# Optimization experiments

Hardware: AMD Instinct MI355X
Metric: run time of the kernel (lower is better)

The kernel has to match this reference:

```python
import jax, jax.numpy as jnp
import numpy as np

B, N, M, D, H, DFF = 1, 2048, 2048, 1024, 16, 4096
MASK_VAL = -50000.0
EPS = 1e-5


def _xavier(k, shape):
    lim = np.sqrt(6.0 / (shape[0] + shape[1])).astype(np.float32)
    return jax.random.uniform(k, shape, jnp.float32, -lim, lim)


def setup_inputs() -> dict:
    key = jax.random.key(0)
    ks = jax.random.split(key, 8)
    return {
        "x": jax.random.normal(ks[0], (B, N, D), jnp.float32),
        "context": jax.random.normal(ks[1], (B, M, D), jnp.float32),
        "Wq": _xavier(ks[2], (D, D)), "bq": jnp.zeros((D,), jnp.float32),
        "Wkv": _xavier(ks[3], (D, 2 * D)), "bkv": jnp.zeros((2 * D,), jnp.float32),
        "Wo": _xavier(ks[4], (D, D)), "bo": jnp.zeros((D,), jnp.float32),
        "ln1_g": jnp.ones((D,), jnp.float32), "ln1_b": jnp.zeros((D,), jnp.float32),
        "W1": _xavier(ks[5], (D, DFF)), "bf1": jnp.zeros((DFF,), jnp.float32),
        "W2": _xavier(ks[6], (DFF, D)), "bf2": jnp.zeros((D,), jnp.float32),
        "ln2_g": jnp.ones((D,), jnp.float32), "ln2_b": jnp.zeros((D,), jnp.float32),
    }


def _layernorm(x, g, b):
    mu = x.mean(-1, keepdims=True)
    var = ((x - mu) ** 2).mean(-1, keepdims=True)
    return (x - mu) * jax.lax.rsqrt(var + EPS) * g + b


def reference(x, context, Wq, bq, Wkv, bkv, Wo, bo, ln1_g, ln1_b, W1, bf1, W2, bf2, ln2_g, ln2_b):
    b, n, d = x.shape
    m = context.shape[1]
    h = H
    dh = d // h
    scale = dh ** -0.5
    # q from x only; k,v from [x; context]
    q = (x @ Wq + bq).reshape(b, n, h, dh).transpose(0, 2, 1, 3)          # b h n dh
    kv_in = jnp.concatenate([x, context], axis=1)                          # b (n+m) d
    k, v = jnp.split(kv_in @ Wkv + bkv, 2, axis=-1)
    k = k.reshape(b, n + m, h, dh).transpose(0, 2, 1, 3)                   # b h (n+m) dh
    v = v.reshape(b, n + m, h, dh).transpose(0, 2, 1, 3)
    dots = jnp.einsum('bhid,bhjd->bhij', q * scale, k)                     # b h n (n+m)
    # causal mask applies only to the self-attention (first n) key columns
    rows = jnp.arange(n)[:, None]
    cols = jnp.arange(n + m)[None, :]
    causal = (cols < n) & (cols > rows)
    dots = jnp.where(causal, MASK_VAL, dots)
    attn = jax.nn.softmax(dots, axis=-1)                                   # dropout = identity (eval)
    out = jnp.einsum('bhij,bhjd->bhid', attn, v)
    out = out.transpose(0, 2, 1, 3).reshape(b, n, d) @ Wo + bo
    # PostNorm(Residual(attn))
    x1 = _layernorm(x + out, ln1_g, ln1_b)
    # PostNorm(Residual(FFN)) with exact-erf GELU
    ff = jax.nn.gelu(x1 @ W1 + bf1, approximate=False) @ W2 + bf2
    return _layernorm(x1 + ff, ln2_g, ln2_b)
```

## Files before the change

kernel.cpp:

```cpp
#include <hip/hip_runtime.h>


using bf16x8 = __attribute__((ext_vector_type(8))) short;
using f32x4  = __attribute__((ext_vector_type(4))) float;

__device__ __forceinline__ ushort f2bf(float f) {
    unsigned u = __float_as_uint(f);
    unsigned r = (u + 0x7fffu + ((u >> 16) & 1u)) >> 16;
    return (ushort)r;
}

__device__ __forceinline__ void gload16(const void* g, void* l) {
    __builtin_amdgcn_global_load_lds(
        (const __attribute__((address_space(1))) void*)g,
        (__attribute__((address_space(3))) void*)l, 16, 0, 0);
}

__device__ __forceinline__ float gelu_erf(float v) {
    return 0.5f * v * (1.0f + erff(v * 0.70710678118654752f));
}

__global__ __launch_bounds__(256) void cvt4(const float* __restrict__ in,
                                            ushort* __restrict__ out, int n) {
    int i = (blockIdx.x * 256 + threadIdx.x) * 4;
    if (i + 3 < n) {
        float4 v = *(const float4*)(in + i);
        ushort4 o;
        o.x = f2bf(v.x); o.y = f2bf(v.y); o.z = f2bf(v.z); o.w = f2bf(v.w);
        *(ushort4*)(out + i) = o;
    }
}

__global__ __launch_bounds__(256) void tcvt(const float* __restrict__ in,
                                            ushort* __restrict__ out, int R, int C) {
    __shared__ float tile[32][33];
    const int tx = threadIdx.x, ty = threadIdx.y;
    const int c0 = blockIdx.x * 32, r0 = blockIdx.y * 32;
#pragma unroll
    for (int i = 0; i < 4; ++i)
        tile[ty + 8 * i][tx] = in[(size_t)(r0 + ty + 8 * i) * C + c0 + tx];
    __syncthreads();
#pragma unroll
    for (int i = 0; i < 4; ++i)
        out[(size_t)(c0 + ty + 8 * i) * R + r0 + tx] = f2bf(tile[tx][ty + 8 * i]);
}

__global__ __launch_bounds__(256) void vtrans(const ushort* __restrict__ KV,
                                              ushort* __restrict__ Vt) {
    __shared__ ushort tile[32][34];
    const int tx = threadIdx.x, ty = threadIdx.y;
    const int j0 = blockIdx.x * 32, d0 = blockIdx.y * 32;
#pragma unroll
    for (int i = 0; i < 4; ++i)
        tile[ty + 8 * i][tx] = KV[(size_t)(j0 + ty + 8 * i) * 2048 + 1024 + d0 + tx];
    __syncthreads();
#pragma unroll
    for (int i = 0; i < 4; ++i)
        Vt[(size_t)(d0 + ty + 8 * i) * 4096 + j0 + tx] = tile[tx][ty + 8 * i];
}

template <int BM, int BN, int ACT, int OUTF32, int RES, int SCALED, int SPLITK>
__global__ __launch_bounds__(256) void gemm_bt(
    const ushort* __restrict__ A, int lda, const ushort* __restrict__ Bt, int ldb,
    const float* __restrict__ bias, const float* __restrict__ resid,
    void* __restrict__ Cout, int M, int N, int K, float scale) {
    constexpr int MR = BM / 32, NR = BN / 32;
    __shared__ __align__(16) ushort Asm[BM * 64];
    __shared__ __align__(16) ushort Bsm[BN * 64];
    const int tid = threadIdx.x;
    const int w = tid >> 6, lane = tid & 63, g = lane >> 4, i15 = lane & 15;
    const int wm = w >> 1, wn = w & 1;
    const int m0 = blockIdx.y * BM, n0 = blockIdx.x * BN;
    if (SPLITK) {
        A += (size_t)blockIdx.z * K;
        Bt += (size_t)blockIdx.z * K;
    }

    f32x4 acc[MR][NR] = {};

    for (int kt = 0; kt < K; kt += 64) {
#pragma unroll
        for (int q = 0; q < BM / 32; ++q) {
            int off = (w * (BM / 32) + q) * 1024 + lane * 16;
            int r = off >> 7, cb = off & 127;
            int scb = cb ^ ((r & 7) << 4);
            const void* src = (const char*)A + ((size_t)(m0 + r) * lda + kt) * 2 + scb;
            gload16(src, (char*)Asm + (w * (BM / 32) + q) * 1024);
        }
#pragma unroll
        for (int q = 0; q < BN / 32; ++q) {
            int off = (w * (BN / 32) + q) * 1024 + lane * 16;
            int r = off >> 7, cb = off & 127;
            int scb = cb ^ ((r & 7) << 4);
            const void* src = (const char*)Bt + ((size_t)(n0 + r) * ldb + kt) * 2 + scb;
            gload16(src, (char*)Bsm + (w * (BN / 32) + q) * 1024);
        }
        __syncthreads();

#pragma unroll
        for (int kc = 0; kc < 2; ++kc) {
            bf16x8 af[MR], bfr[NR];
#pragma unroll
            for (int mi = 0; mi < MR; ++mi) {
                int r = wm * (BM / 2) + mi * 16 + i15;
                af[mi] = *(const bf16x8*)((const char*)Asm + r * 128 +
                                          ((kc * 64 + g * 16) ^ ((r & 7) << 4)));
            }
#pragma unroll
            for (int ni = 0; ni < NR; ++ni) {
                int r = wn * (BN / 2) + ni * 16 + i15;
                bfr[ni] = *(const bf16x8*)((const char*)Bsm + r * 128 +
                                           ((kc * 64 + g * 16) ^ ((r & 7) << 4)));
            }
#pragma unroll
            for (int mi = 0; mi < MR; ++mi)
#pragma unroll
                for (int ni = 0; ni < NR; ++ni)
                    acc[mi][ni] = __builtin_amdgcn_mfma_f32_16x16x32_bf16(
                        af[mi], bfr[ni], acc[mi][ni], 0, 0, 0);
        }
        __syncthreads();
    }

    float* Cf = (float*)Cout;
    if (SPLITK) Cf += (size_t)blockIdx.z * M * N;

#pragma unroll
    for (int ni = 0; ni < NR; ++ni) {
        int col = n0 + wn * (BN / 2) + ni * 16 + i15;
        float bb = bias ? bias[col] : 0.f;
#pragma unroll
        for (int mi = 0; mi < MR; ++mi) {
#pragma unroll
            for (int r2 = 0; r2 < 4; ++r2) {
                int row = m0 + wm * (BM / 2) + mi * 16 + 4 * g + r2;
                float v = acc[mi][ni][r2] + bb;
                if (ACT) v = gelu_erf(v);
                if (SCALED) v *= scale;
                size_t off = (size_t)row * N + col;
                if (OUTF32) {
                    float rv = RES ? resid[off] : 0.f;
                    Cf[off] = v + rv;
                } else {
                    ((ushort*)Cout)[off] = f2bf(v);
                }
            }
        }
    }
}

template <int SPLIT>
__global__ __launch_bounds__(256) void flash_attn(
    const ushort* __restrict__ Q,
    const ushort* __restrict__ KVb,
    const ushort* __restrict__ Vt,
    ushort* __restrict__ O,
    float* __restrict__ Opart,
    float* __restrict__ Ml) {
    constexpr int D = 1024;
    __shared__ __align__(16) ushort Ksm[2][64 * 64];
    __shared__ __align__(16) ushort Vsm[2][64 * 64];
    __shared__ __align__(16) ushort Psm[4][16 * 64];

    const int tid = threadIdx.x;
    const int w = tid >> 6, lane = tid & 63, g = lane >> 4, i15 = lane & 15;
    const int bid = blockIdx.x;
    const int h = bid & 15;
    int qi, s;
    if (SPLIT) { qi = 31 - ((bid >> 4) >> 1); s = (bid >> 4) & 1; }
    else       { qi = 31 - (bid >> 4); s = 0; }
    const int qb = qi * 64;
    const int qrow = qb + w * 16 + i15;

    bf16x8 qf[2];
    qf[0] = *(const bf16x8*)(Q + (size_t)qrow * D + h * 64 + g * 8);
    qf[1] = *(const bf16x8*)(Q + (size_t)qrow * D + h * 64 + 32 + g * 8);

    f32x4 o[4] = {};
    float m_run = -INFINITY, l_run = 0.f;

    const int diag = qi;
    const int nt = diag + 33;
    const int lo = (SPLIT && s) ? (nt >> 1) : 0;
    const int hi = SPLIT ? (s ? nt : (nt >> 1)) : nt;

    const int sr  = tid >> 3;
    const int scb = (tid & 7) * 16;
    const int ssw = scb ^ ((sr & 7) << 4);
    const char* kb0 = (const char*)KVb + ((size_t)sr * 2048 + h * 64) * 2 + scb;
    const char* vb0 = (const char*)Vt + ((size_t)(h * 64 + sr) * 4096) * 2 + scb;

    uint4 kreg0, kreg1, vreg0, vreg1;
    auto jt_of = [&](int t) { return (t <= diag) ? t : (32 + (t - diag - 1)); };
    auto stage = [&](int jt) {
        const char* kb = kb0 + (size_t)jt * 64 * 2048 * 2;
        kreg0 = *(const uint4*)kb;
        kreg1 = *(const uint4*)(kb + 32 * 2048 * 2);
        const char* vb = vb0 + (size_t)jt * 64 * 2;
        vreg0 = *(const uint4*)vb;
        vreg1 = *(const uint4*)(vb + 32 * 4096 * 2);
    };
    auto wlds = [&](int buf) {
        *(uint4*)((char*)Ksm[buf] + sr * 128 + ssw) = kreg0;
        *(uint4*)((char*)Ksm[buf] + (sr + 32) * 128 + ssw) = kreg1;
        *(uint4*)((char*)Vsm[buf] + sr * 128 + ssw) = vreg0;
        *(uint4*)((char*)Vsm[buf] + (sr + 32) * 128 + ssw) = vreg1;
    };

    stage(jt_of(lo));
    wlds(0);
    __syncthreads();
    int cur = 0;

    const int pbase = i15 * 128;
    const int psw = (i15 & 7) << 4;

    for (int t = lo; t < hi; ++t) {
        const int jt = jt_of(t);
        const bool more = (t + 1 < hi);
        if (more) stage(jt_of(t + 1));

        f32x4 st[4];
#pragma unroll
        for (int jg = 0; jg < 4; ++jg) {
            int jr = jg * 16 + i15;
            bf16x8 ka0 = *(const bf16x8*)((const char*)Ksm[cur] + jr * 128 +
                                          ((g * 16) ^ ((jr & 7) << 4)));
            bf16x8 ka1 = *(const bf16x8*)((const char*)Ksm[cur] + jr * 128 +
                                          ((64 + g * 16) ^ ((jr & 7) << 4)));
            f32x4 z = {};
            z = __builtin_amdgcn_mfma_f32_16x16x32_bf16(ka0, qf[0], z, 0, 0, 0);
            z = __builtin_amdgcn_mfma_f32_16x16x32_bf16(ka1, qf[1], z, 0, 0, 0);
            st[jg] = z;
        }
        if (jt == diag) {
#pragma unroll
            for (int jg = 0; jg < 4; ++jg)
#pragma unroll
                for (int r = 0; r < 4; ++r) {
                    int j = jt * 64 + jg * 16 + 4 * g + r;
                    if (j > qrow) st[jg][r] = -50000.f;
                }
        }

        float mt = -INFINITY;
#pragma unroll
        for (int jg = 0; jg < 4; ++jg)
#pragma unroll
            for (int r = 0; r < 4; ++r) mt = fmaxf(mt, st[jg][r]);
        mt = fmaxf(mt, __shfl_xor(mt, 16));
        mt = fmaxf(mt, __shfl_xor(mt, 32));

        const bool skip = __all(mt - m_run <= 8.f);
        float mnew, fscale;
        if (skip) { mnew = m_run; fscale = 1.f; }
        else      { mnew = fmaxf(m_run, mt); fscale = exp2f(m_run - mnew); }

        float psum = 0.f;
        float pf[4][4];
#pragma unroll
        for (int jg = 0; jg < 4; ++jg)
#pragma unroll
            for (int r = 0; r < 4; ++r) {
                float p = exp2f(st[jg][r] - mnew);
                psum += p;
                pf[jg][r] = p;
            }
        psum += __shfl_xor(psum, 16);
        psum += __shfl_xor(psum, 32);
        l_run = l_run * fscale + psum;
        m_run = mnew;

        if (!skip) {
#pragma unroll
            for (int r = 0; r < 4; ++r) {
                float fr = __shfl(fscale, 20 * g + r);
#pragma unroll
                for (int dg = 0; dg < 4; ++dg) o[dg][r] *= fr;
            }
        }

#pragma unroll
        for (int jg = 0; jg < 4; ++jg) {
            uint pk0, pk1;
            asm("v_cvt_pk_bf16_f32 %0, %1, %2" : "=v"(pk0) : "v"(pf[jg][0]), "v"(pf[jg][1]));
            asm("v_cvt_pk_bf16_f32 %0, %1, %2" : "=v"(pk1) : "v"(pf[jg][2]), "v"(pf[jg][3]));
            uint2 pk; pk.x = pk0; pk.y = pk1;
            *(uint2*)((char*)Psm[w] + pbase + ((jg * 32 + g * 8) ^ psw)) = pk;
        }

#pragma unroll
        for (int jc = 0; jc < 2; ++jc) {
            bf16x8 pa = *(const bf16x8*)((const char*)Psm[w] + pbase +
                                         ((jc * 64 + g * 16) ^ psw));
#pragma unroll
            for (int dg = 0; dg < 4; ++dg) {
                int dr = dg * 16 + i15;
                bf16x8 vb = *(const bf16x8*)((const char*)Vsm[cur] + dr * 128 +
                                             ((jc * 64 + g * 16) ^ ((dr & 7) << 4)));
                o[dg] = __builtin_amdgcn_mfma_f32_16x16x32_bf16(pa, vb, o[dg], 0, 0, 0);
            }
        }

        if (more) wlds(cur ^ 1);
        __syncthreads();
        cur ^= 1;
    }

    if (SPLIT) {
        if (g == 0) {
            float* mp = Ml + ((size_t)(s * 2048 + qb + w * 16 + i15) * 16 + h) * 2;
            mp[0] = m_run; mp[1] = l_run;
        }
#pragma unroll
        for (int r = 0; r < 4; ++r)
#pragma unroll
            for (int dg = 0; dg < 4; ++dg) {
                int row = qb + w * 16 + 4 * g + r;
                int col = h * 64 + dg * 16 + i15;
                Opart[(size_t)(s * 2048 + row) * 1024 + col] = o[dg][r];
            }
    } else {
#pragma unroll
        for (int r = 0; r < 4; ++r) {
            float lr = __shfl(l_run, 20 * g + r);
            float inv = 1.f / lr;
#pragma unroll
            for (int dg = 0; dg < 4; ++dg) {
                int row = qb + w * 16 + 4 * g + r;
                int col = h * 64 + dg * 16 + i15;
                O[(size_t)row * D + col] = f2bf(o[dg][r] * inv);
            }
        }
    }
}

__global__ __launch_bounds__(256) void attn_combine(
    const float* __restrict__ Opart, const float* __restrict__ Ml,
    ushort* __restrict__ O) {
    const int row = blockIdx.x, tid = threadIdx.x;
    const int c = tid * 4, h = c >> 6;
    const float* mp0 = Ml + ((size_t)row * 16 + h) * 2;
    const float* mp1 = Ml + ((size_t)(2048 + row) * 16 + h) * 2;
    float m0 = mp0[0], l0 = mp0[1], m1 = mp1[0], l1 = mp1[1];
    float m = fmaxf(m0, m1);
    float w0 = exp2f(m0 - m), w1 = exp2f(m1 - m);
    float inv = 1.f / (l0 * w0 + l1 * w1);
    float4 a = *(const float4*)(Opart + (size_t)row * 1024 + c);
    float4 b = *(const float4*)(Opart + (size_t)(2048 + row) * 1024 + c);
    ushort4 ob;
    ob.x = f2bf((a.x * w0 + b.x * w1) * inv);
    ob.y = f2bf((a.y * w0 + b.y * w1) * inv);
    ob.z = f2bf((a.z * w0 + b.z * w1) * inv);
    ob.w = f2bf((a.w * w0 + b.w * w1) * inv);
    *(ushort4*)(O + (size_t)row * 1024 + c) = ob;
}

__global__ __launch_bounds__(256) void layernorm_k(
    const float* __restrict__ in, const float* __restrict__ gam,
    const float* __restrict__ bet, float* __restrict__ outf,
    ushort* __restrict__ outb) {
    const int row = blockIdx.x, tid = threadIdx.x;
    const float4 v = *(const float4*)(in + (size_t)row * 1024 + tid * 4);
    float s = v.x + v.y + v.z + v.w;
    float sq = v.x * v.x + v.y * v.y + v.z * v.z + v.w * v.w;
#pragma unroll
    for (int d = 1; d < 64; d <<= 1) {
        s += __shfl_xor(s, d);
        sq += __shfl_xor(sq, d);
    }
    __shared__ float red[8];
    const int w = tid >> 6;
    if ((tid & 63) == 0) { red[w] = s; red[4 + w] = sq; }
    __syncthreads();
    s = red[0] + red[1] + red[2] + red[3];
    sq = red[4] + red[5] + red[6] + red[7];
    const float mu = s * (1.f / 1024.f);
    const float rs = rsqrtf(sq * (1.f / 1024.f) - mu * mu + 1e-5f);
    const float4 gg = *(const float4*)(gam + tid * 4);
    const float4 bb = *(const float4*)(bet + tid * 4);
    float4 o;
    o.x = (v.x - mu) * rs * gg.x + bb.x;
    o.y = (v.y - mu) * rs * gg.y + bb.y;
    o.z = (v.z - mu) * rs * gg.z + bb.z;
    o.w = (v.w - mu) * rs * gg.w + bb.w;
    *(float4*)(outf + (size_t)row * 1024 + tid * 4) = o;
    if (outb) {
        ushort4 ob;
        ob.x = f2bf(o.x); ob.y = f2bf(o.y); ob.z = f2bf(o.z); ob.w = f2bf(o.w);
        *(ushort4*)(outb + (size_t)row * 1024 + tid * 4) = ob;
    }
}

__global__ __launch_bounds__(256) void layernorm_comb(
    const float* __restrict__ in0, const float* __restrict__ in1,
    const float* __restrict__ bias, const float* __restrict__ resid,
    const float* __restrict__ gam, const float* __restrict__ bet,
    float* __restrict__ outf) {
    const int row = blockIdx.x, tid = threadIdx.x;
    const float4 a = *(const float4*)(in0 + (size_t)row * 1024 + tid * 4);
    const float4 b = *(const float4*)(in1 + (size_t)row * 1024 + tid * 4);
    const float4 rr = *(const float4*)(resid + (size_t)row * 1024 + tid * 4);
    const float4 bs = *(const float4*)(bias + tid * 4);
    float4 v;
    v.x = a.x + b.x + rr.x + bs.x;
    v.y = a.y + b.y + rr.y + bs.y;
    v.z = a.z + b.z + rr.z + bs.z;
    v.w = a.w + b.w + rr.w + bs.w;
    float s = v.x + v.y + v.z + v.w;
    float sq = v.x * v.x + v.y * v.y + v.z * v.z + v.w * v.w;
#pragma unroll
    for (int d = 1; d < 64; d <<= 1) {
        s += __shfl_xor(s, d);
        sq += __shfl_xor(sq, d);
    }
    __shared__ float red[8];
    const int w = tid >> 6;
    if ((tid & 63) == 0) { red[w] = s; red[4 + w] = sq; }
    __syncthreads();
    s = red[0] + red[1] + red[2] + red[3];
    sq = red[4] + red[5] + red[6] + red[7];
    const float mu = s * (1.f / 1024.f);
    const float rs = rsqrtf(sq * (1.f / 1024.f) - mu * mu + 1e-5f);
    const float4 gg = *(const float4*)(gam + tid * 4);
    const float4 bb = *(const float4*)(bet + tid * 4);
    float4 o;
    o.x = (v.x - mu) * rs * gg.x + bb.x;
    o.y = (v.y - mu) * rs * gg.y + bb.y;
    o.z = (v.z - mu) * rs * gg.z + bb.z;
    o.w = (v.w - mu) * rs * gg.w + bb.w;
    *(float4*)(outf + (size_t)row * 1024 + tid * 4) = o;
}

extern "C" void kernel_launch(void* const* d_in, const int* in_sizes, int n_in,
                              void* d_out, int out_size, void* d_ws, size_t ws_size,
                              hipStream_t stream) {
    const float* x    = (const float*)d_in[0];
    const float* ctx  = (const float*)d_in[1];
    const float* Wq   = (const float*)d_in[2];
    const float* bq   = (const float*)d_in[3];
    const float* Wkv  = (const float*)d_in[4];
    const float* bkv  = (const float*)d_in[5];
    const float* Wo   = (const float*)d_in[6];
    const float* bo   = (const float*)d_in[7];
    const float* g1   = (const float*)d_in[8];
    const float* b1   = (const float*)d_in[9];
    const float* W1   = (const float*)d_in[10];
    const float* bf1  = (const float*)d_in[11];
    const float* W2   = (const float*)d_in[12];
    const float* bf2  = (const float*)d_in[13];
    const float* g2   = (const float*)d_in[14];
    const float* b2   = (const float*)d_in[15];

    char* ws = (char*)d_ws;
    const size_t MB = 1u << 20;
    ushort* XCb  = (ushort*)(ws + 0);
    ushort* WoT  = (ushort*)(ws + 8 * MB);
    ushort* W1T  = (ushort*)(ws + 10 * MB);
    ushort* W2T  = (ushort*)(ws + 18 * MB);
    ushort* WqT  = (ushort*)(ws + 26 * MB);
    ushort* WkvT = (ushort*)(ws + 28 * MB);
    ushort* Qs   = (ushort*)(ws + 32 * MB);
    ushort* attn = (ushort*)(ws + 36 * MB);
    ushort* KV   = (ushort*)(ws + 40 * MB);
    ushort* Vt   = (ushort*)(ws + 56 * MB);
    ushort* x1b  = (ushort*)(ws + 26 * MB);
    float*  x1f  = (float*)(ws + 32 * MB);
    ushort* ffb  = (ushort*)(ws + 40 * MB);
    float*  y1   = (float*)(ws + 56 * MB);
    float*  Pk   = (float*)(ws + 0);
    float*  Opart = (float*)(ws + 64 * MB);
    float*  Ml    = (float*)(ws + 80 * MB);
    const bool split = ws_size >= 81 * MB;

    cvt4<<<2048, 256, 0, stream>>>(x, XCb, 2048 * 1024);
    cvt4<<<2048, 256, 0, stream>>>(ctx, XCb + 2048 * 1024, 2048 * 1024);
    tcvt<<<dim3(32, 32), dim3(32, 8), 0, stream>>>(Wq, WqT, 1024, 1024);
    tcvt<<<dim3(64, 32), dim3(32, 8), 0, stream>>>(Wkv, WkvT, 1024, 2048);
    tcvt<<<dim3(32, 32), dim3(32, 8), 0, stream>>>(Wo, WoT, 1024, 1024);
    tcvt<<<dim3(128, 32), dim3(32, 8), 0, stream>>>(W1, W1T, 1024, 4096);
    tcvt<<<dim3(32, 128), dim3(32, 8), 0, stream>>>(W2, W2T, 4096, 1024);
    gemm_bt<64, 128, 0, 0, 0, 1, 0><<<dim3(8, 32), 256, 0, stream>>>(
        XCb, 1024, WqT, 1024, bq, nullptr, Qs, 2048, 1024, 1024, 0.18033688011112042f);
    gemm_bt<128, 128, 0, 0, 0, 0, 0><<<dim3(16, 32), 256, 0, stream>>>(
        XCb, 1024, WkvT, 1024, bkv, nullptr, KV, 4096, 2048, 1024, 1.f);
    vtrans<<<dim3(128, 32), dim3(32, 8), 0, stream>>>(KV, Vt);
    if (split) {
        flash_attn<1><<<1024, 256, 0, stream>>>(Qs, KV, Vt, nullptr, Opart, Ml);
        attn_combine<<<2048, 256, 0, stream>>>(Opart, Ml, attn);
    } else {
        flash_attn<0><<<512, 256, 0, stream>>>(Qs, KV, Vt, attn, nullptr, nullptr);
    }
    gemm_bt<64, 128, 0, 1, 1, 0, 0><<<dim3(8, 32), 256, 0, stream>>>(
        attn, 1024, WoT, 1024, bo, x, y1, 2048, 1024, 1024, 1.f);
    layernorm_k<<<2048, 256, 0, stream>>>(y1, g1, b1, x1f, x1b);
    gemm_bt<128, 128, 1, 0, 0, 0, 0><<<dim3(32, 16), 256, 0, stream>>>(
        x1b, 1024, W1T, 1024, bf1, nullptr, ffb, 2048, 4096, 1024, 1.f);
    gemm_bt<64, 128, 0, 1, 0, 0, 1><<<dim3(8, 32, 2), 256, 0, stream>>>(
        ffb, 4096, W2T, 4096, nullptr, nullptr, Pk, 2048, 1024, 2048, 1.f);
    layernorm_comb<<<2048, 256, 0, stream>>>(Pk, Pk + 2048 * 1024, bf2, x1f,
                                             g2, b2, (float*)d_out);
}
```

Before: 236.8 us.

## Rewrite flash attention with 32x32 MFMA, register-resident K/V and 4-way KV split

Replaces the 16x16 MFMA flash-attention kernel with one that uses 32x32x16 bf16 MFMA, gives each wave 32 query rows, and loads K and V fragments straight from global memory into registers, with no LDS staging or block barriers. P is moved into the B-operand layout with permlane32_swap instead of an LDS round trip. The KV range is split 4 ways (falling back to 2 or 1 depending on workspace size), and the combine kernel is generalised to NS partials. Several smaller GEMMs also switch from 128 to 64 column tiles to launch more blocks. The risks are higher register pressure and redundant global K/V loads across waves, plus more partial-output traffic in the combine step.

```diff
diff --git a/kernel.cpp b/kernel.cpp
--- a/kernel.cpp
+++ b/kernel.cpp
@@ -3,6 +3,7 @@
 
 using bf16x8 = __attribute__((ext_vector_type(8))) short;
 using f32x4  = __attribute__((ext_vector_type(4))) float;
+using f32x16 = __attribute__((ext_vector_type(16))) float;
 
 __device__ __forceinline__ ushort f2bf(float f) {
     unsigned u = __float_as_uint(f);
@@ -18,6 +19,16 @@
 
 __device__ __forceinline__ float gelu_erf(float v) {
     return 0.5f * v * (1.0f + erff(v * 0.70710678118654752f));
+}
+
+__device__ __forceinline__ f32x16 mfma32(bf16x8 a, bf16x8 b, f32x16 c) {
+    return __builtin_amdgcn_mfma_f32_32x32x16_bf16(a, b, c, 0, 0, 0);
+}
+
+__device__ __forceinline__ uint cvtpk(float a, float b) {
+    uint r;
+    asm("v_cvt_pk_bf16_f32 %0, %1, %2" : "=v"(r) : "v"(a), "v"(b));
+    return r;
 }
 
 __global__ __launch_bounds__(256) void cvt4(const float* __restrict__ in,
@@ -149,106 +160,87 @@
     }
 }
 
-template <int SPLIT>
-__global__ __launch_bounds__(256) void flash_attn(
+template <int NS>
+__global__ __launch_bounds__(256) void flash_attn2(
     const ushort* __restrict__ Q,
     const ushort* __restrict__ KVb,
     const ushort* __restrict__ Vt,
     ushort* __restrict__ O,
     float* __restrict__ Opart,
     float* __restrict__ Ml) {
-    constexpr int D = 1024;
-    __shared__ __align__(16) ushort Ksm[2][64 * 64];
-    __shared__ __align__(16) ushort Vsm[2][64 * 64];
-    __shared__ __align__(16) ushort Psm[4][16 * 64];
-
     const int tid = threadIdx.x;
-    const int w = tid >> 6, lane = tid & 63, g = lane >> 4, i15 = lane & 15;
+    const int w = tid >> 6, lane = tid & 63;
+    const int i31 = lane & 31, hig = lane >> 5;
     const int bid = blockIdx.x;
     const int h = bid & 15;
-    int qi, s;
-    if (SPLIT) { qi = 31 - ((bid >> 4) >> 1); s = (bid >> 4) & 1; }
-    else       { qi = 31 - (bid >> 4); s = 0; }
-    const int qb = qi * 64;
-    const int qrow = qb + w * 16 + i15;
-
-    bf16x8 qf[2];
-    qf[0] = *(const bf16x8*)(Q + (size_t)qrow * D + h * 64 + g * 8);
-    qf[1] = *(const bf16x8*)(Q + (size_t)qrow * D + h * 64 + 32 + g * 8);
-
-    f32x4 o[4] = {};
+    const int qB = 15 - ((bid >> 4) & 15);
+    const int s = bid >> 8;
+    const int qb = qB * 128 + w * 32;
+    const int qrow = qb + i31;
+    const int diag = qb >> 6;
+    const int nt = diag + 33;
+    const int lo = (s * nt) / NS;
+    const int ht = ((s + 1) * nt) / NS;
+
+    bf16x8 qf[4], kf[8], vf[8];
+    {
+        const ushort* qp = Q + (size_t)qrow * 1024 + h * 64 + hig * 8;
+#pragma unroll
+        for (int ks = 0; ks < 4; ++ks) qf[ks] = *(const bf16x8*)(qp + ks * 16);
+    }
+    const ushort* kb_p = KVb + h * 64 + hig * 8;
+    const ushort* vb_p = Vt + (size_t)(h * 64 + i31) * 4096 + hig * 8;
+
+    auto load_k = [&](int jt) {
+#pragma unroll
+        for (int sub = 0; sub < 2; ++sub)
+#pragma unroll
+            for (int ks = 0; ks < 4; ++ks)
+                kf[sub * 4 + ks] = *(const bf16x8*)(
+                    kb_p + (size_t)(jt * 64 + sub * 32 + i31) * 2048 + ks * 16);
+    };
+    auto load_v = [&](int jt) {
+#pragma unroll
+        for (int ds = 0; ds < 2; ++ds)
+#pragma unroll
+            for (int t4 = 0; t4 < 4; ++t4)
+                vf[ds * 4 + t4] = *(const bf16x8*)(
+                    vb_p + (size_t)ds * 32 * 4096 + jt * 64 + t4 * 16);
+    };
+
+    f32x16 o0 = {}, o1 = {};
     float m_run = -INFINITY, l_run = 0.f;
 
-    const int diag = qi;
-    const int nt = diag + 33;
-    const int lo = (SPLIT && s) ? (nt >> 1) : 0;
-    const int hi = SPLIT ? (s ? nt : (nt >> 1)) : nt;
-
-    const int sr  = tid >> 3;
-    const int scb = (tid & 7) * 16;
-    const int ssw = scb ^ ((sr & 7) << 4);
-    const char* kb0 = (const char*)KVb + ((size_t)sr * 2048 + h * 64) * 2 + scb;
-    const char* vb0 = (const char*)Vt + ((size_t)(h * 64 + sr) * 4096) * 2 + scb;
-
-    uint4 kreg0, kreg1, vreg0, vreg1;
-    auto jt_of = [&](int t) { return (t <= diag) ? t : (32 + (t - diag - 1)); };
-    auto stage = [&](int jt) {
-        const char* kb = kb0 + (size_t)jt * 64 * 2048 * 2;
-        kreg0 = *(const uint4*)kb;
-        kreg1 = *(const uint4*)(kb + 32 * 2048 * 2);
-        const char* vb = vb0 + (size_t)jt * 64 * 2;
-        vreg0 = *(const uint4*)vb;
-        vreg1 = *(const uint4*)(vb + 32 * 4096 * 2);
-    };
-    auto wlds = [&](int buf) {
-        *(uint4*)((char*)Ksm[buf] + sr * 128 + ssw) = kreg0;
-        *(uint4*)((char*)Ksm[buf] + (sr + 32) * 128 + ssw) = kreg1;
-        *(uint4*)((char*)Vsm[buf] + sr * 128 + ssw) = vreg0;
-        *(uint4*)((char*)Vsm[buf] + (sr + 32) * 128 + ssw) = vreg1;
-    };
-
-    stage(jt_of(lo));
-    wlds(0);
-    __syncthreads();
-    int cur = 0;
-
-    const int pbase = i15 * 128;
-    const int psw = (i15 & 7) << 4;
-
-    for (int t = lo; t < hi; ++t) {
-        const int jt = jt_of(t);
-        const bool more = (t + 1 < hi);
-        if (more) stage(jt_of(t + 1));
-
-        f32x4 st[4];
-#pragma unroll
-        for (int jg = 0; jg < 4; ++jg) {
-            int jr = jg * 16 + i15;
-            bf16x8 ka0 = *(const bf16x8*)((const char*)Ksm[cur] + jr * 128 +
-                                          ((g * 16) ^ ((jr & 7) << 4)));
-            bf16x8 ka1 = *(const bf16x8*)((const char*)Ksm[cur] + jr * 128 +
-                                          ((64 + g * 16) ^ ((jr & 7) << 4)));
-            f32x4 z = {};
-            z = __builtin_amdgcn_mfma_f32_16x16x32_bf16(ka0, qf[0], z, 0, 0, 0);
-            z = __builtin_amdgcn_mfma_f32_16x16x32_bf16(ka1, qf[1], z, 0, 0, 0);
-            st[jg] = z;
-        }
-        if (jt == diag) {
-#pragma unroll
-            for (int jg = 0; jg < 4; ++jg)
-#pragma unroll
-                for (int r = 0; r < 4; ++r) {
-                    int j = jt * 64 + jg * 16 + 4 * g + r;
-                    if (j > qrow) st[jg][r] = -50000.f;
-                }
+    {
+        int jt0 = (lo <= diag) ? lo : 32 + (lo - diag - 1);
+        load_k(jt0);
+        load_v(jt0);
+    }
+
+    for (int t = lo; t < ht; ++t) {
+        const int tn = (t + 1 < ht) ? t + 1 : t;
+        const int jtn = (tn <= diag) ? tn : 32 + (tn - diag - 1);
+
+        f32x16 s0 = {}, s1 = {};
+#pragma unroll
+        for (int ks = 0; ks < 4; ++ks) s0 = mfma32(kf[ks], qf[ks], s0);
+#pragma unroll
+        for (int ks = 0; ks < 4; ++ks) s1 = mfma32(kf[4 + ks], qf[ks], s1);
+        load_k(jtn);
+
+        if (t == diag) {
+            const int jb = diag * 64;
+#pragma unroll
+            for (int r = 0; r < 16; ++r) {
+                int jl = (r & 3) + 8 * (r >> 2) + 4 * hig;
+                if (jb + jl > qrow) s0[r] = -50000.f;
+                if (jb + 32 + jl > qrow) s1[r] = -50000.f;
+            }
         }
 
         float mt = -INFINITY;
 #pragma unroll
-        for (int jg = 0; jg < 4; ++jg)
-#pragma unroll
-            for (int r = 0; r < 4; ++r) mt = fmaxf(mt, st[jg][r]);
-        mt = fmaxf(mt, __shfl_xor(mt, 16));
+        for (int r = 0; r < 16; ++r) mt = fmaxf(mt, fmaxf(s0[r], s1[r]));
         mt = fmaxf(mt, __shfl_xor(mt, 32));
 
         const bool skip = __all(mt - m_run <= 8.f);
@@ -257,102 +249,108 @@
         else      { mnew = fmaxf(m_run, mt); fscale = exp2f(m_run - mnew); }
 
         float psum = 0.f;
-        float pf[4][4];
-#pragma unroll
-        for (int jg = 0; jg < 4; ++jg)
-#pragma unroll
-            for (int r = 0; r < 4; ++r) {
-                float p = exp2f(st[jg][r] - mnew);
-                psum += p;
-                pf[jg][r] = p;
-            }
-        psum += __shfl_xor(psum, 16);
+#pragma unroll
+        for (int r = 0; r < 16; ++r) {
+            s0[r] = exp2f(s0[r] - mnew);
+            s1[r] = exp2f(s1[r] - mnew);
+            psum += s0[r] + s1[r];
+        }
         psum += __shfl_xor(psum, 32);
         l_run = l_run * fscale + psum;
         m_run = mnew;
 
         if (!skip) {
 #pragma unroll
-            for (int r = 0; r < 4; ++r) {
-                float fr = __shfl(fscale, 20 * g + r);
-#pragma unroll
-                for (int dg = 0; dg < 4; ++dg) o[dg][r] *= fr;
-            }
-        }
-
-#pragma unroll
-        for (int jg = 0; jg < 4; ++jg) {
-            uint pk0, pk1;
-            asm("v_cvt_pk_bf16_f32 %0, %1, %2" : "=v"(pk0) : "v"(pf[jg][0]), "v"(pf[jg][1]));
-            asm("v_cvt_pk_bf16_f32 %0, %1, %2" : "=v"(pk1) : "v"(pf[jg][2]), "v"(pf[jg][3]));
-            uint2 pk; pk.x = pk0; pk.y = pk1;
-            *(uint2*)((char*)Psm[w] + pbase + ((jg * 32 + g * 8) ^ psw)) = pk;
-        }
-
-#pragma unroll
-        for (int jc = 0; jc < 2; ++jc) {
-            bf16x8 pa = *(const bf16x8*)((const char*)Psm[w] + pbase +
-                                         ((jc * 64 + g * 16) ^ psw));
-#pragma unroll
-            for (int dg = 0; dg < 4; ++dg) {
-                int dr = dg * 16 + i15;
-                bf16x8 vb = *(const bf16x8*)((const char*)Vsm[cur] + dr * 128 +
-                                             ((jc * 64 + g * 16) ^ ((dr & 7) << 4)));
-                o[dg] = __builtin_amdgcn_mfma_f32_16x16x32_bf16(pa, vb, o[dg], 0, 0, 0);
-            }
-        }
-
-        if (more) wlds(cur ^ 1);
-        __syncthreads();
-        cur ^= 1;
-    }
-
-    if (SPLIT) {
-        if (g == 0) {
-            float* mp = Ml + ((size_t)(s * 2048 + qb + w * 16 + i15) * 16 + h) * 2;
+            for (int r = 0; r < 16; ++r) { o0[r] *= fscale; o1[r] *= fscale; }
+        }
+
+#pragma unroll
+        for (int t4 = 0; t4 < 4; ++t4) {
+            const int r0 = 8 * (t4 & 1);
+            uint w0, w1, w2, w3;
+            if (t4 < 2) {
+                w0 = cvtpk(s0[r0 + 0], s0[r0 + 1]);
+                w1 = cvtpk(s0[r0 + 2], s0[r0 + 3]);
+                w2 = cvtpk(s0[r0 + 4], s0[r0 + 5]);
+                w3 = cvtpk(s0[r0 + 6], s0[r0 + 7]);
+            } else {
+                w0 = cvtpk(s1[r0 + 0], s1[r0 + 1]);
+                w1 = cvtpk(s1[r0 + 2], s1[r0 + 3]);
+                w2 = cvtpk(s1[r0 + 4], s1[r0 + 5]);
+                w3 = cvtpk(s1[r0 + 6], s1[r0 + 7]);
+            }
+            asm volatile("v_permlane32_swap_b32 %0, %1" : "+v"(w0), "+v"(w2));
+            asm volatile("v_permlane32_swap_b32 %0, %1" : "+v"(w1), "+v"(w3));
+            uint4 pw; pw.x = w0; pw.y = w1; pw.z = w2; pw.w = w3;
+            bf16x8 pfr = *(bf16x8*)&pw;
+            o0 = mfma32(vf[t4], pfr, o0);
+            o1 = mfma32(vf[4 + t4], pfr, o1);
+        }
+        load_v(jtn);
+    }
+
+    if (NS == 1) {
+        float inv = 1.f / l_run;
+#pragma unroll
+        for (int ds = 0; ds < 2; ++ds)
+#pragma unroll
+            for (int q = 0; q < 4; ++q) {
+                float v0 = (ds ? o1[4 * q + 0] : o0[4 * q + 0]) * inv;
+                float v1 = (ds ? o1[4 * q + 1] : o0[4 * q + 1]) * inv;
+                float v2 = (ds ? o1[4 * q + 2] : o0[4 * q + 2]) * inv;
+                float v3 = (ds ? o1[4 * q + 3] : o0[4 * q + 3]) * inv;
+                uint2 pk; pk.x = cvtpk(v0, v1); pk.y = cvtpk(v2, v3);
+                int col = h * 64 + ds * 32 + 8 * q + 4 * hig;
+                *(uint2*)(O + (size_t)qrow * 1024 + col) = pk;
+            }
+    } else {
+        if (hig == 0) {
+            float* mp = Ml + ((size_t)(s * 2048 + qrow) * 16 + h) * 2;
             mp[0] = m_run; mp[1] = l_run;
         }
 #pragma unroll
-        for (int r = 0; r < 4; ++r)
-#pragma unroll
-            for (int dg = 0; dg < 4; ++dg) {
-                int row = qb + w * 16 + 4 * g + r;
-                int col = h * 64 + dg * 16 + i15;
-                Opart[(size_t)(s * 2048 + row) * 1024 + col] = o[dg][r];
-            }
-    } else {
-#pragma unroll
-        for (int r = 0; r < 4; ++r) {
-            float lr = __shfl(l_run, 20 * g + r);
-            float inv = 1.f / lr;
-#pragma unroll
-            for (int dg = 0; dg < 4; ++dg) {
-                int row = qb + w * 16 + 4 * g + r;
-                int col = h * 64 + dg * 16 + i15;
-                O[(size_t)row * D + col] = f2bf(o[dg][r] * inv);
-            }
-        }
-    }
-}
-
+        for (int ds = 0; ds < 2; ++ds)
+#pragma unroll
+            for (int q = 0; q < 4; ++q) {
+                float4 v;
+                v.x = ds ? o1[4 * q + 0] : o0[4 * q + 0];
+                v.y = ds ? o1[4 * q + 1] : o0[4 * q + 1];
+                v.z = ds ? o1[4 * q + 2] : o0[4 * q + 2];
+                v.w = ds ? o1[4 * q + 3] : o0[4 * q + 3];
+                int col = h * 64 + ds * 32 + 8 * q + 4 * hig;
+                *(float4*)(Opart + (size_t)(s * 2048 + qrow) * 1024 + col) = v;
+            }
+    }
+}
+
+template <int NS>
 __global__ __launch_bounds__(256) void attn_combine(
     const float* __restrict__ Opart, const float* __restrict__ Ml,
     ushort* __restrict__ O) {
     const int row = blockIdx.x, tid = threadIdx.x;
     const int c = tid * 4, h = c >> 6;
-    const float* mp0 = Ml + ((size_t)row * 16 + h) * 2;
-    const float* mp1 = Ml + ((size_t)(2048 + row) * 16 + h) * 2;
-    float m0 = mp0[0], l0 = mp0[1], m1 = mp1[0], l1 = mp1[1];
-    float m = fmaxf(m0, m1);
-    float w0 = exp2f(m0 - m), w1 = exp2f(m1 - m);
-    float inv = 1.f / (l0 * w0 + l1 * w1);
-    float4 a = *(const float4*)(Opart + (size_t)row * 1024 + c);
-    float4 b = *(const float4*)(Opart + (size_t)(2048 + row) * 1024 + c);
+    float ms[NS], ls[NS];
+#pragma unroll
+    for (int s = 0; s < NS; ++s) {
+        const float* mp = Ml + ((size_t)(s * 2048 + row) * 16 + h) * 2;
+        ms[s] = mp[0]; ls[s] = mp[1];
+    }
+    float m = ms[0];
+#pragma unroll
+    for (int s = 1; s < NS; ++s) m = fmaxf(m, ms[s]);
+    float denom = 0.f, wgt[NS];
+#pragma unroll
+    for (int s = 0; s < NS; ++s) { wgt[s] = exp2f(ms[s] - m); denom += ls[s] * wgt[s]; }
+    const float inv = 1.f / denom;
+    float ax = 0, ay = 0, az = 0, aw = 0;
+#pragma unroll
+    for (int s = 0; s < NS; ++s) {
+        float4 a = *(const float4*)(Opart + (size_t)(s * 2048 + row) * 1024 + c);
+        ax += a.x * wgt[s]; ay += a.y * wgt[s]; az += a.z * wgt[s]; aw += a.w * wgt[s];
+    }
     ushort4 ob;
-    ob.x = f2bf((a.x * w0 + b.x * w1) * inv);
-    ob.y = f2bf((a.y * w0 + b.y * w1) * inv);
-    ob.z = f2bf((a.z * w0 + b.z * w1) * inv);
-    ob.w = f2bf((a.w * w0 + b.w * w1) * inv);
+    ob.x = f2bf(ax * inv); ob.y = f2bf(ay * inv);
+    ob.z = f2bf(az * inv); ob.w = f2bf(aw * inv);
     *(ushort4*)(O + (size_t)row * 1024 + c) = ob;
 }
 
@@ -470,8 +468,6 @@
     float*  y1   = (float*)(ws + 56 * MB);
     float*  Pk   = (float*)(ws + 0);
     float*  Opart = (float*)(ws + 64 * MB);
-    float*  Ml    = (float*)(ws + 80 * MB);
-    const bool split = ws_size >= 81 * MB;
 
     cvt4<<<2048, 256, 0, stream>>>(x, XCb, 2048 * 1024);
     cvt4<<<2048, 256, 0, stream>>>(ctx, XCb + 2048 * 1024, 2048 * 1024);
@@ -480,23 +476,32 @@
     tcvt<<<dim3(32, 32), dim3(32, 8), 0, stream>>>(Wo, WoT, 1024, 1024);
     tcvt<<<dim3(128, 32), dim3(32, 8), 0, stream>>>(W1, W1T, 1024, 4096);
     tcvt<<<dim3(32, 128), dim3(32, 8), 0, stream>>>(W2, W2T, 4096, 1024);
-    gemm_bt<64, 128, 0, 0, 0, 1, 0><<<dim3(8, 32), 256, 0, stream>>>(
+    gemm_bt<64, 64, 0, 0, 0, 1, 0><<<dim3(16, 32), 256, 0, stream>>>(
         XCb, 1024, WqT, 1024, bq, nullptr, Qs, 2048, 1024, 1024, 0.18033688011112042f);
     gemm_bt<128, 128, 0, 0, 0, 0, 0><<<dim3(16, 32), 256, 0, stream>>>(
         XCb, 1024, WkvT, 1024, bkv, nullptr, KV, 4096, 2048, 1024, 1.f);
     vtrans<<<dim3(128, 32), dim3(32, 8), 0, stream>>>(KV, Vt);
-    if (split) {
-        flash_attn<1><<<1024, 256, 0, stream>>>(Qs, KV, Vt, nullptr, Opart, Ml);
-        attn_combine<<<2048, 256, 0, stream>>>(Opart, Ml, attn);
+
+    const size_t need4 = 64 * MB + 4 * 8 * MB + 4 * 2048 * 16 * 2 * 4;
+    const size_t need2 = 64 * MB + 2 * 8 * MB + 2 * 2048 * 16 * 2 * 4;
+    if (ws_size >= need4) {
+        float* Ml = Opart + (size_t)4 * 2048 * 1024;
+        flash_attn2<4><<<1024, 256, 0, stream>>>(Qs, KV, Vt, nullptr, Opart, Ml);
+        attn_combine<4><<<2048, 256, 0, stream>>>(Opart, Ml, attn);
+    } else if (ws_size >= need2) {
+        float* Ml = Opart + (size_t)2 * 2048 * 1024;
+        flash_attn2<2><<<512, 256, 0, stream>>>(Qs, KV, Vt, nullptr, Opart, Ml);
+        attn_combine<2><<<2048, 256, 0, stream>>>(Opart, Ml, attn);
     } else {
-        flash_attn<0><<<512, 256, 0, stream>>>(Qs, KV, Vt, attn, nullptr, nullptr);
-    }
-    gemm_bt<64, 128, 0, 1, 1, 0, 0><<<dim3(8, 32), 256, 0, stream>>>(
+        flash_attn2<1><<<256, 256, 0, stream>>>(Qs, KV, Vt, attn, nullptr, nullptr);
+    }
+
+    gemm_bt<64, 64, 0, 1, 1, 0, 0><<<dim3(16, 32), 256, 0, stream>>>(
         attn, 1024, WoT, 1024, bo, x, y1, 2048, 1024, 1024, 1.f);
     layernorm_k<<<2048, 256, 0, stream>>>(y1, g1, b1, x1f, x1b);
     gemm_bt<128, 128, 1, 0, 0, 0, 0><<<dim3(32, 16), 256, 0, stream>>>(
         x1b, 1024, W1T, 1024, bf1, nullptr, ffb, 2048, 4096, 1024, 1.f);
-    gemm_bt<64, 128, 0, 1, 0, 0, 1><<<dim3(8, 32, 2), 256, 0, stream>>>(
+    gemm_bt<64, 64, 0, 1, 0, 0, 1><<<dim3(16, 32, 2), 256, 0, stream>>>(
         ffb, 4096, W2T, 4096, nullptr, nullptr, Pk, 2048, 1024, 2048, 1.f);
     layernorm_comb<<<2048, 256, 0, stream>>>(Pk, Pk + 2048 * 1024, bf2, x1f,
                                              g2, b2, (float*)d_out);
```

After: 277.1 us. 1.17x slower.
